# Optimization experiments

Measured on AMD Instinct MI355X. Metric: run time of the kernel, lower is better.

Reference implementation:

```python
import jax, jax.numpy as jnp
import numpy as np

N_CELLS = 65536
NH = 7
NV = 4
E_IN = 16
E_OUT = 16
N_OFF = 4
N_SIG = 4
B = 2


def setup_inputs() -> dict:
    key = jax.random.key(0)
    ks = jax.random.split(key, 8)
    x = jax.random.normal(ks[0], (B, N_CELLS, NV, E_IN), dtype=jnp.float32)
    # coords[0]=lat in [-pi/2, pi/2], coords[1]=lon in [-pi, pi]
    lat = (jax.random.uniform(ks[1], (N_CELLS,), dtype=jnp.float32) - 0.5) * jnp.pi
    lon = (jax.random.uniform(ks[2], (N_CELLS,), dtype=jnp.float32) - 0.5) * 2 * jnp.pi
    coords = jnp.stack([lat, lon], axis=0)
    # positive sigmas / offsets on the scale of typical grid distances
    sigma = jax.random.uniform(ks[3], (N_SIG,), dtype=jnp.float32) * 0.5 + 0.05
    dist_offsets = jax.random.uniform(ks[4], (N_OFF,), dtype=jnp.float32) * 0.5
    W = jax.random.normal(ks[5], (N_OFF, N_SIG, E_IN, E_OUT), dtype=jnp.float32) / np.sqrt(N_OFF * N_SIG * E_IN)
    b_out = jnp.zeros((E_OUT,), dtype=jnp.float32)
    adjc = jax.random.randint(ks[6], (N_CELLS, NH), 0, N_CELLS, dtype=jnp.int32)
    nh_mask = jax.random.randint(ks[7], (N_CELLS, NH), 0, 2, dtype=jnp.int32)
    return {"x": x, "coords": coords, "sigma": sigma, "dist_offsets": dist_offsets,
            "W": W, "b_out": b_out, "adjc": adjc, "nh_mask": nh_mask}


def _polar_distance(lat_c, lon_c, lat_nh, lon_nh):
    # great-circle distance (radians) between center cell and its neighbors
    dlon = lon_nh - lon_c
    cosd = (jnp.sin(lat_c) * jnp.sin(lat_nh)
            + jnp.cos(lat_c) * jnp.cos(lat_nh) * jnp.cos(dlon))
    return jnp.arccos(jnp.clip(cosd, -1.0 + 1e-7, 1.0 - 1e-7))  # [n, nh]


def reference(x, coords, sigma, dist_offsets, W, b_out, adjc, nh_mask):
    # neighborhood coordinate gather: [n, nh]
    lat, lon = coords[0], coords[1]
    lat_nh, lon_nh = lat[adjc], lon[adjc]
    d = _polar_distance(lat[:, None], lon[:, None], lat_nh, lon_nh)  # [n, nh]
    # Gaussian (RBF) kernel over distance offsets x sigmas: normal_dist with sigma_cross
    diff = d[:, :, None] - dist_offsets  # [n, nh, o]
    nd = jnp.exp(-0.5 * (diff[..., None] / sigma) ** 2)  # [n, nh, o, s]
    nd = nd * nh_mask.astype(nd.dtype)[:, :, None, None]
    nd = nd / (nd.sum(axis=1, keepdims=True) + 1e-8)  # normalize over neighborhood
    # multi-level neighbor feature gather: [b, n, nh, nv, e]
    x_nh = x[:, adjc]
    # RBF-weighted neighborhood aggregation: [b, n, o, s, nv, e]
    agg = jnp.einsum('bnhve,nhos->bnosve', x_nh, nd)
    # projection over (offset, sigma, e_in) -> e_out: [b, n, nv, e_out]
    out = jnp.einsum('bnosve,osef->bnvf', agg, W) + b_out
    return out
```

## Files before the change

kernel.cpp:

```cpp
#include <hip/hip_runtime.h>
#include <hip/hip_bf16.h>
#include <math.h>

#define N_CELLS 65536
#define NH 7
#define NV 4
#define E_IN 16
#define E_OUT 16
#define NK 16

#define CPB 32
#define THREADS 256
#define TRP 20

typedef __attribute__((ext_vector_type(8))) short bf16x8;
typedef __attribute__((ext_vector_type(4))) float f32x4;
typedef __attribute__((ext_vector_type(2))) float f32x2;
typedef unsigned long long u64;

#define NDOFF(k, cl) (((k) << 8) + ((((cl) ^ ((k) & 3))) << 3))

#define WAIT_LGKM0 0xC07F

static __device__ __forceinline__ short f2bfs(float f) {
    __hip_bfloat16 h = __float2bfloat16(f);
    short s;
    __builtin_memcpy(&s, &h, 2);
    return s;
}

__global__ __launch_bounds__(256) void setup_kernel(
    const float* __restrict__ x, const float* __restrict__ coords,
    const float* __restrict__ W,
    short* __restrict__ wf, unsigned char* __restrict__ xq, float* __restrict__ meta)
{
    const int t = threadIdx.x;
    const int g = blockIdx.x * 64 + (t >> 2);
    const int p = t & 3;

    const float4* src = (const float4*)(x + (size_t)g * 64 + p * 16);
    float4 q[4];
    #pragma unroll
    for (int i = 0; i < 4; ++i) q[i] = src[i];

    float amax = 0.0f;
    #pragma unroll
    for (int i = 0; i < 4; ++i)
        amax = fmaxf(amax, fmaxf(fmaxf(fabsf(q[i].x), fabsf(q[i].y)),
                                 fmaxf(fabsf(q[i].z), fabsf(q[i].w))));
    amax = fmaxf(amax, __shfl_xor(amax, 1));
    amax = fmaxf(amax, __shfl_xor(amax, 2));
    amax = fmaxf(amax, 1e-12f);

    const float inv = 127.0f / amax;
    const float s   = amax / 127.0f;

    unsigned int w[4];
    #pragma unroll
    for (int i = 0; i < 4; ++i) {
        const float vs[4] = {q[i].x, q[i].y, q[i].z, q[i].w};
        unsigned int ww = 0;
        #pragma unroll
        for (int j = 0; j < 4; ++j) {
            float r = rintf(vs[j] * inv);
            r = fminf(fmaxf(r, -127.0f), 127.0f);
            ww |= ((unsigned int)(int)(r + 128.0f) & 0xffu) << (8 * j);
        }
        w[i] = ww;
    }
    const int cell = g & (N_CELLS - 1);
    const int b    = g >> 16;
    *(uint4*)(xq + (size_t)cell * 128 + b * 64 + p * 16) = make_uint4(w[0], w[1], w[2], w[3]);

    if (p == 0) meta[(size_t)cell * 8 + 4 + b] = s;

    if (p == 0 && b == 0) {
        const float lat = coords[cell];
        const float lon = coords[N_CELLS + cell];
        meta[(size_t)cell * 8 + 0] = sinf(lat);
        meta[(size_t)cell * 8 + 1] = cosf(lat);
        meta[(size_t)cell * 8 + 2] = sinf(lon);
        meta[(size_t)cell * 8 + 3] = cosf(lon);
        meta[(size_t)cell * 8 + 6] = 0.0f;
        meta[(size_t)cell * 8 + 7] = 0.0f;
    }

    if (blockIdx.x == 0) {
        const int kk  = t;
        const int j   = kk & 7;
        const int grp = (kk >> 3) & 3;
        const int st  = kk >> 5;
        #pragma unroll
        for (int col = 0; col < E_OUT; ++col)
            wf[(((st * 4 + grp) * 16) + col) * 8 + j] = f2bfs(W[kk * E_OUT + col]);
    }
}

__global__ __launch_bounds__(THREADS, 3) void mge_kernel(
    const unsigned char* __restrict__ xq,
    const float* __restrict__ meta,
    const float* __restrict__ sigma,
    const float* __restrict__ dist_offsets,
    const short* __restrict__ wf,
    const float* __restrict__ b_out,
    const int*   __restrict__ adjc,
    const int*   __restrict__ nh_mask,
    float* __restrict__ out)
{
    __shared__ float nd_flat[2][NK * 256];
    __shared__ int   adj_lds[CPB][NH];
    __shared__ float d_lds[CPB][NH];
    __shared__ float m_lds[CPB][NH];
    __shared__ float scl_lds[CPB][NH][2];
    __shared__ float tr_lds[4][16][TRP];

    const int t    = threadIdx.x;
    const int lane = t & 63;
    const int wv   = t >> 6;
    const int base = blockIdx.x * CPB;

    if (t < CPB * NH) {
        const int cl = t / NH;
        const int h  = t % NH;
        const int n  = base + cl;
        const int a  = adjc[n * NH + h];
        const int m  = nh_mask[n * NH + h];
        adj_lds[cl][h] = a;
        const float4 gc = *(const float4*)(meta + (size_t)n * 8);
        const float4 gn = *(const float4*)(meta + (size_t)a * 8);
        const float2 sn = *(const float2*)(meta + (size_t)a * 8 + 4);
        const float cdl = gn.w * gc.w + gn.z * gc.z;
        float cosd = gc.x * gn.x + gc.y * gn.y * cdl;
        cosd = fminf(fmaxf(cosd, -1.0f + 1e-7f), 1.0f - 1e-7f);
        d_lds[cl][h] = acosf(cosd);
        m_lds[cl][h] = (float)m;
        scl_lds[cl][h][0] = sn.x;
        scl_lds[cl][h][1] = sn.y;
    }

    const int col = lane & 15;
    const int grp = lane >> 4;
    bf16x8 bfrag[8];
    #pragma unroll
    for (int st = 0; st < 8; ++st)
        bfrag[st] = ((const bf16x8*)wf)[(st * 4 + grp) * 16 + col];
    const float obias = b_out[col];

    __syncthreads();

    const int arow = lane & 15;
    const int cq   = arow >> 2;
    const int v    = arow & 3;
    const int e0   = (grp & 1) * 8;
    const int kos_off = grp >> 1;

    u64 xbA[NH], xbB[NH];

#define LOADQ(XB, Q)                                                            \
    {                                                                           \
        const int cl_ = (wv << 3) + (((Q) & 1) << 2) + cq;                      \
        const int b_  = (Q) >> 1;                                               \
        _Pragma("unroll")                                                       \
        for (int h = 0; h < NH; ++h) {                                          \
            const int a = adj_lds[cl_][h];                                      \
            XB[h] = *(const u64*)(xq + (size_t)a * 128 + (b_ << 6) + (v << 4) + e0); \
        }                                                                       \
    }

    LOADQ(xbA, 0)
    LOADQ(xbB, 1)

    #pragma unroll
    for (int it = 0; it < 2; ++it) {
        const int task = it * THREADS + t;
        const int cl = task >> 4;
        const int k  = task & 15;
        const int o  = k >> 2;
        const int s  = k & 3;
        const float off     = dist_offsets[o];
        const float inv_sig = 1.0f / sigma[s];
        float raw[NH];
        float sum = 0.0f;
        #pragma unroll
        for (int h = 0; h < NH; ++h) {
            const float df = (d_lds[cl][h] - off) * inv_sig;
            const float e  = __expf(-0.5f * df * df) * m_lds[cl][h];
            raw[h] = e;
            sum += e;
        }
        const float inv = 1.0f / (sum + 1e-8f);
        float nd0[NH], nd1[NH];
        float cb0 = 0.0f, cb1 = 0.0f;
        #pragma unroll
        for (int h = 0; h < NH; ++h) {
            const float nd = raw[h] * inv;
            nd0[h] = nd * scl_lds[cl][h][0];
            nd1[h] = nd * scl_lds[cl][h][1];
            cb0 += nd0[h];
            cb1 += nd1[h];
        }
        float* dst0 = &nd_flat[0][NDOFF(k, cl)];
        *(f32x4*)dst0       = (f32x4){nd0[0], nd0[1], nd0[2], nd0[3]};
        *(f32x4*)(dst0 + 4) = (f32x4){nd0[4], nd0[5], nd0[6], -128.0f * cb0};
        float* dst1 = &nd_flat[1][NDOFF(k, cl)];
        *(f32x4*)dst1       = (f32x4){nd1[0], nd1[1], nd1[2], nd1[3]};
        *(f32x4*)(dst1 + 4) = (f32x4){nd1[4], nd1[5], nd1[6], -128.0f * cb1};
    }
    __syncthreads();

#define COMPQ(XB, Q)                                                            \
    {                                                                           \
        const int cl_ = (wv << 3) + (((Q) & 1) << 2) + cq;                      \
        const int b_  = (Q) >> 1;                                               \
               \
        f32x2 u2[NH][4];                                                        \
        _Pragma("unroll")                                                       \
        for (int h = 0; h < NH; ++h) {                                          \
            const unsigned lo = (unsigned)XB[h], hi = (unsigned)(XB[h] >> 32);  \
            u2[h][0] = (f32x2){(float)(lo & 0xffu), (float)((lo >> 8) & 0xffu)};  \
            u2[h][1] = (f32x2){(float)((lo >> 16) & 0xffu), (float)(lo >> 24)};   \
            u2[h][2] = (f32x2){(float)(hi & 0xffu), (float)((hi >> 8) & 0xffu)};  \
            u2[h][3] = (f32x2){(float)((hi >> 16) & 0xffu), (float)(hi >> 24)};   \
        }                                                                       \
        const float* ndbase = nd_flat[b_];                                      \
        f32x4 acc = {0.f, 0.f, 0.f, 0.f};                                       \
        _Pragma("unroll")                                                       \
        for (int st = 0; st < 8; ++st) {                                        \
            const int k2 = st * 2 + kos_off;                                    \
            const float* ndp = ndbase + NDOFF(k2, cl_);                         \
            const f32x4 n0 = *(const f32x4*)ndp;                                \
            const f32x4 n1 = *(const f32x4*)(ndp + 4);                          \
            const float nds[NH] = {n0.x, n0.y, n0.z, n0.w, n1.x, n1.y, n1.z};   \
            const float ng = n1.w;                                              \
            f32x2 s0 = {ng, ng}, s1 = {ng, ng};                                 \
            f32x2 s2 = {ng, ng}, s3 = {ng, ng};                                 \
            _Pragma("unroll")                                                   \
            for (int h = 0; h < NH; ++h) {                                      \
                const f32x2 nd2 = {nds[h], nds[h]};                             \
                s0 = __builtin_elementwise_fma(nd2, u2[h][0], s0);              \
                s1 = __builtin_elementwise_fma(nd2, u2[h][1], s1);              \
                s2 = __builtin_elementwise_fma(nd2, u2[h][2], s2);              \
                s3 = __builtin_elementwise_fma(nd2, u2[h][3], s3);              \
            }                                                                   \
            bf16x8 aa;                                                          \
            aa[0] = f2bfs(s0.x); aa[1] = f2bfs(s0.y);                           \
            aa[2] = f2bfs(s1.x); aa[3] = f2bfs(s1.y);                           \
            aa[4] = f2bfs(s2.x); aa[5] = f2bfs(s2.y);                           \
            aa[6] = f2bfs(s3.x); aa[7] = f2bfs(s3.y);                           \
            acc = __builtin_amdgcn_mfma_f32_16x16x32_bf16(aa, bfrag[st], acc, 0, 0, 0); \
        }                                                                       \
            \
        _Pragma("unroll")                                                       \
        for (int r = 0; r < 4; ++r)                                             \
            tr_lds[wv][grp * 4 + r][col] = acc[r] + obias;                      \
        __builtin_amdgcn_s_waitcnt(WAIT_LGKM0);                                 \
        __builtin_amdgcn_sched_barrier(0);                                      \
        {                                                                       \
            const int rr = lane >> 2;                                           \
            const int cc = (lane & 3) << 2;                                     \
            const f32x4 val = *(const f32x4*)&tr_lds[wv][rr][cc];               \
            const size_t qbase = ((size_t)b_ << 16) + base + (wv << 3) + (((Q) & 1) << 2); \
            __builtin_nontemporal_store(val, (f32x4*)(out + qbase * 64 + rr * 16 + cc)); \
        }                                                                       \
    }

    COMPQ(xbA, 0)
    LOADQ(xbA, 2)
    COMPQ(xbB, 1)
    LOADQ(xbB, 3)
    COMPQ(xbA, 2)
    COMPQ(xbB, 3)

#undef LOADQ
#undef COMPQ
}

extern "C" void kernel_launch(void* const* d_in, const int* in_sizes, int n_in,
                              void* d_out, int out_size, void* d_ws, size_t ws_size,
                              hipStream_t stream) {
    const float* x            = (const float*)d_in[0];
    const float* coords       = (const float*)d_in[1];
    const float* sigma        = (const float*)d_in[2];
    const float* dist_offsets = (const float*)d_in[3];
    const float* W            = (const float*)d_in[4];
    const float* b_out        = (const float*)d_in[5];
    const int*   adjc         = (const int*)d_in[6];
    const int*   nh_mask      = (const int*)d_in[7];
    float* out = (float*)d_out;

    char* ws = (char*)d_ws;
    short*         wf   = (short*)ws;
    float*         meta = (float*)(ws + 8192);
    unsigned char* xq   = (unsigned char*)(ws + 8192 + 2097152);

    setup_kernel<<<2048, 256, 0, stream>>>(x, coords, W, wf, xq, meta);
    dim3 grid(N_CELLS / CPB);
    mge_kernel<<<grid, THREADS, 0, stream>>>(xq, meta, sigma, dist_offsets,
                                             wf, b_out, adjc, nh_mask, out);
}
```

Baseline: 48.77 us.

## Apply per-batch dequant scale to x in registers and share one nd table

The normalized RBF weights are now stored once in LDS instead of twice (once per batch with the quantization scale folded in). The per-batch scale and zero-point are applied to the dequantized x values in registers before the neighborhood FMA loop. This halves the nd LDS footprint and raises the launch-bounds occupancy hint from 3 to 5 blocks per CU. The cost is extra FMAs per neighbor in the dequant step and a tighter register budget from the higher occupancy target, which may cause spills.

```diff
diff --git a/kernel.cpp b/kernel.cpp
--- a/kernel.cpp
+++ b/kernel.cpp
@@ -96,7 +96,7 @@
     }
 }
 
-__global__ __launch_bounds__(THREADS, 3) void mge_kernel(
+__global__ __launch_bounds__(THREADS, 5) void mge_kernel(
     const unsigned char* __restrict__ xq,
     const float* __restrict__ meta,
     const float* __restrict__ sigma,
@@ -107,7 +107,7 @@
     const int*   __restrict__ nh_mask,
     float* __restrict__ out)
 {
-    __shared__ float nd_flat[2][NK * 256];
+    __shared__ float nd_flat[NK * 256];
     __shared__ int   adj_lds[CPB][NH];
     __shared__ float d_lds[CPB][NH];
     __shared__ float m_lds[CPB][NH];
@@ -189,22 +189,9 @@
             sum += e;
         }
         const float inv = 1.0f / (sum + 1e-8f);
-        float nd0[NH], nd1[NH];
-        float cb0 = 0.0f, cb1 = 0.0f;
-        #pragma unroll
-        for (int h = 0; h < NH; ++h) {
-            const float nd = raw[h] * inv;
-            nd0[h] = nd * scl_lds[cl][h][0];
-            nd1[h] = nd * scl_lds[cl][h][1];
-            cb0 += nd0[h];
-            cb1 += nd1[h];
-        }
-        float* dst0 = &nd_flat[0][NDOFF(k, cl)];
-        *(f32x4*)dst0       = (f32x4){nd0[0], nd0[1], nd0[2], nd0[3]};
-        *(f32x4*)(dst0 + 4) = (f32x4){nd0[4], nd0[5], nd0[6], -128.0f * cb0};
-        float* dst1 = &nd_flat[1][NDOFF(k, cl)];
-        *(f32x4*)dst1       = (f32x4){nd1[0], nd1[1], nd1[2], nd1[3]};
-        *(f32x4*)(dst1 + 4) = (f32x4){nd1[4], nd1[5], nd1[6], -128.0f * cb1};
+        float* dst = nd_flat + NDOFF(k, cl);
+        *(f32x4*)dst       = (f32x4){raw[0] * inv, raw[1] * inv, raw[2] * inv, raw[3] * inv};
+        *(f32x4*)(dst + 4) = (f32x4){raw[4] * inv, raw[5] * inv, raw[6] * inv, 0.0f};
     }
     __syncthreads();
 
@@ -212,35 +199,42 @@
     {                                                                           \
         const int cl_ = (wv << 3) + (((Q) & 1) << 2) + cq;                      \
         const int b_  = (Q) >> 1;                                               \
-               \
-        f32x2 u2[NH][4];                                                        \
+                       \
+        f32x2 xf2[NH][4];                                                       \
         _Pragma("unroll")                                                       \
         for (int h = 0; h < NH; ++h) {                                          \
+            const float sc = scl_lds[cl_][h][b_];                               \
+            const float nb = -128.0f * sc;                                      \
+            const f32x2 sc2 = {sc, sc};                                         \
+            const f32x2 nb2 = {nb, nb};                                         \
             const unsigned lo = (unsigned)XB[h], hi = (unsigned)(XB[h] >> 32);  \
-            u2[h][0] = (f32x2){(float)(lo & 0xffu), (float)((lo >> 8) & 0xffu)};  \
-            u2[h][1] = (f32x2){(float)((lo >> 16) & 0xffu), (float)(lo >> 24)};   \
-            u2[h][2] = (f32x2){(float)(hi & 0xffu), (float)((hi >> 8) & 0xffu)};  \
-            u2[h][3] = (f32x2){(float)((hi >> 16) & 0xffu), (float)(hi >> 24)};   \
-        }                                                                       \
-        const float* ndbase = nd_flat[b_];                                      \
+            f32x2 u;                                                            \
+            u = (f32x2){(float)(lo & 0xffu), (float)((lo >> 8) & 0xffu)};       \
+            xf2[h][0] = __builtin_elementwise_fma(u, sc2, nb2);                 \
+            u = (f32x2){(float)((lo >> 16) & 0xffu), (float)(lo >> 24)};        \
+            xf2[h][1] = __builtin_elementwise_fma(u, sc2, nb2);                 \
+            u = (f32x2){(float)(hi & 0xffu), (float)((hi >> 8) & 0xffu)};       \
+            xf2[h][2] = __builtin_elementwise_fma(u, sc2, nb2);                 \
+            u = (f32x2){(float)((hi >> 16) & 0xffu), (float)(hi >> 24)};        \
+            xf2[h][3] = __builtin_elementwise_fma(u, sc2, nb2);                 \
+        }                                                                       \
         f32x4 acc = {0.f, 0.f, 0.f, 0.f};                                       \
         _Pragma("unroll")                                                       \
         for (int st = 0; st < 8; ++st) {                                        \
             const int k2 = st * 2 + kos_off;                                    \
-            const float* ndp = ndbase + NDOFF(k2, cl_);                         \
+            const float* ndp = nd_flat + NDOFF(k2, cl_);                        \
             const f32x4 n0 = *(const f32x4*)ndp;                                \
             const f32x4 n1 = *(const f32x4*)(ndp + 4);                          \
             const float nds[NH] = {n0.x, n0.y, n0.z, n0.w, n1.x, n1.y, n1.z};   \
-            const float ng = n1.w;                                              \
-            f32x2 s0 = {ng, ng}, s1 = {ng, ng};                                 \
-            f32x2 s2 = {ng, ng}, s3 = {ng, ng};                                 \
+            f32x2 s0 = {0.f, 0.f}, s1 = {0.f, 0.f};                             \
+            f32x2 s2 = {0.f, 0.f}, s3 = {0.f, 0.f};                             \
             _Pragma("unroll")                                                   \
             for (int h = 0; h < NH; ++h) {                                      \
                 const f32x2 nd2 = {nds[h], nds[h]};                             \
-                s0 = __builtin_elementwise_fma(nd2, u2[h][0], s0);              \
-                s1 = __builtin_elementwise_fma(nd2, u2[h][1], s1);              \
-                s2 = __builtin_elementwise_fma(nd2, u2[h][2], s2);              \
-                s3 = __builtin_elementwise_fma(nd2, u2[h][3], s3);              \
+                s0 = __builtin_elementwise_fma(nd2, xf2[h][0], s0);             \
+                s1 = __builtin_elementwise_fma(nd2, xf2[h][1], s1);             \
+                s2 = __builtin_elementwise_fma(nd2, xf2[h][2], s2);             \
+                s3 = __builtin_elementwise_fma(nd2, xf2[h][3], s3);             \
             }                                                                   \
             bf16x8 aa;                                                          \
             aa[0] = f2bfs(s0.x); aa[1] = f2bfs(s0.y);                           \
```

Measured after the change: 100.3 us. 2.06x slower.
